# Performance work log

Hardware: AMD Instinct MI355X
Metric: run time of the kernel (lower is better)

The kernel has to match this reference:

```python
import jax, jax.numpy as jnp
import numpy as np

B, N, NE = 2, 10000, 320000
ND, ED = 128, 128
EPS = 1e-5


def _mlp(x, w1, b1, w2, b2, g, beta):
    # Linear -> SiLU -> Linear -> LayerNorm (MLP with n_hidden=1, layer_norm=True)
    h = jax.nn.silu(x @ w1 + b1)
    y = h @ w2 + b2
    mu = jnp.mean(y, axis=-1, keepdims=True)
    var = jnp.mean((y - mu) ** 2, axis=-1, keepdims=True)
    return (y - mu) * jax.lax.rsqrt(var + EPS) * g + beta


def setup_inputs() -> dict:
    key = jax.random.key(0)
    ks = jax.random.split(key, 16)
    V = jax.random.normal(ks[0], (B, N, ND), dtype=jnp.float32)
    E = jax.random.normal(ks[1], (B, NE, ED), dtype=jnp.float32)
    edges = jax.random.randint(ks[2], (B, NE, 2), 0, N, dtype=jnp.int32)
    inv = jax.random.bernoulli(ks[3], 0.01, (B, NE, 1))
    edges = jnp.where(inv, jnp.int32(-1), edges)

    def lin(k, fan_in, fan_out):
        kw, kb = jax.random.split(k)
        lim = 1.0 / np.sqrt(fan_in)
        w = jax.random.uniform(kw, (fan_in, fan_out), jnp.float32, -lim, lim)
        b = jax.random.uniform(kb, (fan_out,), jnp.float32, -lim, lim)
        return w, b

    fe_w1, fe_b1 = lin(ks[4], 2 * ND + ED, ND)   # f_edge: hidden=node_dim
    fe_w2, fe_b2 = lin(ks[5], ND, ED)
    fn_w1, fn_b1 = lin(ks[6], ND + ED, ND)       # f_node: hidden=node_dim
    fn_w2, fn_b2 = lin(ks[7], ND, ND)
    return {
        "V": V, "E": E, "edges": edges,
        "fe_w1": fe_w1, "fe_b1": fe_b1, "fe_w2": fe_w2, "fe_b2": fe_b2,
        "fe_g": jnp.ones((ED,), jnp.float32), "fe_beta": jnp.zeros((ED,), jnp.float32),
        "fn_w1": fn_w1, "fn_b1": fn_b1, "fn_w2": fn_w2, "fn_b2": fn_b2,
        "fn_g": jnp.ones((ND,), jnp.float32), "fn_beta": jnp.zeros((ND,), jnp.float32),
    }


def reference(V, E, edges, fe_w1, fe_b1, fe_w2, fe_b2, fe_g, fe_beta,
              fn_w1, fn_b1, fn_w2, fn_b2, fn_g, fn_beta):
    valid = jnp.all(edges >= 0, axis=-1)              # [B, NE]
    safe = jnp.clip(edges, 0, N - 1)                  # [B, NE, 2]
    bidx = jnp.arange(B)[:, None]
    S = V[bidx, safe[..., 0]]                         # [B, NE, ND] gather senders
    R = V[bidx, safe[..., 1]]                         # [B, NE, ND] gather receivers
    e_new = _mlp(jnp.concatenate([S, R, E], axis=-1), fe_w1, fe_b1, fe_w2, fe_b2, fe_g, fe_beta)
    e_new = e_new * valid[..., None]

    # scatter_mean over receiver index (invalid edges still counted, clamped to idx 0,
    # contributing zeros — matches torch scatter_mean with count.clamp(min=1))
    seg = (safe[..., 1] + bidx * N).reshape(-1)       # [B*NE]
    sums = jax.ops.segment_sum(e_new.reshape(-1, ED), seg, num_segments=B * N)
    cnt = jax.ops.segment_sum(jnp.ones((B * NE,), jnp.float32), seg, num_segments=B * N)
    agg = (sums / jnp.maximum(cnt, 1.0)[:, None]).reshape(B, N, ED)

    v_new = _mlp(jnp.concatenate([V, agg], axis=-1), fn_w1, fn_b1, fn_w2, fn_b2, fn_g, fn_beta)
    return V + v_new, E + e_new
```

## Files before the change

kernel.cpp:

```cpp
#include <hip/hip_runtime.h>

typedef float f32x4 __attribute__((ext_vector_type(4)));
typedef __bf16 bf16x8 __attribute__((ext_vector_type(8)));

constexpr int BATCH = 2;
constexpr int NNODE = 10000;
constexpr int NEDGE = 320000;
constexpr int D = 128;

constexpr size_t WS_SUMS = 0;
constexpr size_t WS_CNT  = 10240000;
constexpr size_t WS_W1E  = 10320000;
constexpr size_t WS_W2E  = 10418304;
constexpr size_t WS_W1N  = 10451072;
constexpr size_t WS_W2N  = 10516608;

__device__ __forceinline__ f32x4 mfma16(bf16x8 a, bf16x8 b, f32x4 c) {
    return __builtin_amdgcn_mfma_f32_16x16x32_bf16(a, b, c, 0, 0, 0);
}
__device__ __forceinline__ __bf16 tobf(float x) { return (__bf16)x; }
__device__ __forceinline__ bf16x8 cvt8(float4 a, float4 b) {
    bf16x8 r;
    r[0]=tobf(a.x); r[1]=tobf(a.y); r[2]=tobf(a.z); r[3]=tobf(a.w);
    r[4]=tobf(b.x); r[5]=tobf(b.y); r[6]=tobf(b.z); r[7]=tobf(b.w);
    return r;
}
__device__ __forceinline__ bf16x8 cvt8s(float4 a, float4 b, float s) {
    bf16x8 r;
    r[0]=tobf(a.x*s); r[1]=tobf(a.y*s); r[2]=tobf(a.z*s); r[3]=tobf(a.w*s);
    r[4]=tobf(b.x*s); r[5]=tobf(b.y*s); r[6]=tobf(b.z*s); r[7]=tobf(b.w*s);
    return r;
}
__device__ __forceinline__ float silu(float x) {
    float t = __builtin_amdgcn_exp2f(x * -1.44269504f);
    return x * __builtin_amdgcn_rcpf(1.0f + t);
}

__global__ void gnn_pack_kernel(const float* __restrict__ fe_w1, const float* __restrict__ fe_w2,
                                const float* __restrict__ fn_w1, const float* __restrict__ fn_w2,
                                ushort* __restrict__ w1e, ushort* __restrict__ w2e,
                                ushort* __restrict__ w1n, ushort* __restrict__ w2n) {
    int t = blockIdx.x * blockDim.x + threadIdx.x;
    const float* src; ushort* dst; int lt;
    if      (t <  6144) { src = fe_w1; dst = w1e; lt = t;         }
    else if (t <  8192) { src = fe_w2; dst = w2e; lt = t - 6144;  }
    else if (t < 12288) { src = fn_w1; dst = w1n; lt = t - 8192;  }
    else if (t < 14336) { src = fn_w2; dst = w2n; lt = t - 12288; }
    else return;
    int lane = lt & 63, ct = (lt >> 6) & 7, kb = lt >> 9;
    int n  = ct * 16 + (lane & 15);
    int k0 = kb * 32 + (lane >> 4) * 8;
    ushort tmp[8];
#pragma unroll
    for (int j = 0; j < 8; j++)
        tmp[j] = __builtin_bit_cast(ushort, tobf(src[(size_t)(k0 + j) * 128 + n]));
    uint4 pk;
    pk.x = tmp[0] | ((uint)tmp[1] << 16); pk.y = tmp[2] | ((uint)tmp[3] << 16);
    pk.z = tmp[4] | ((uint)tmp[5] << 16); pk.w = tmp[6] | ((uint)tmp[7] << 16);
    *(uint4*)(dst + (size_t)lt * 8) = pk;
}

__global__ void gnn_cnt_kernel(const int* __restrict__ edges, unsigned* __restrict__ cnt) {
    int t = blockIdx.x * blockDim.x + threadIdx.x;
    if (t >= BATCH * NEDGE) return;
    int er = edges[2 * t + 1];
    int b  = (t >= NEDGE) ? 1 : 0;
    int r  = min(max(er, 0), NNODE - 1);
    atomicAdd(&cnt[b * NNODE + r], 1u);
}

__launch_bounds__(512, 2)
__global__ void gnn_edge_kernel(const float* __restrict__ V, const float* __restrict__ E,
                                const int* __restrict__ edges,
                                const float* __restrict__ b1, const float* __restrict__ b2,
                                const float* __restrict__ g, const float* __restrict__ beta,
                                const ushort* __restrict__ w1p, const ushort* __restrict__ w2p,
                                float* __restrict__ sums, float* __restrict__ E_out) {
    __shared__ __align__(16) ushort lds[(98304 + 32768) / 2];
    const int tid = threadIdx.x;
    const int wave = tid >> 6, lane = tid & 63;
    const int quad = lane >> 4, c16 = lane & 15;

    {
        const uint4* s4 = (const uint4*)w1p;
        uint4* d4 = (uint4*)lds;
#pragma unroll
        for (int i = 0; i < 12; i++) d4[tid + i * 512] = s4[tid + i * 512];
    }
    __syncthreads();

    float b1v[8], b2v[8], gv[8], bev[8];
#pragma unroll
    for (int ct = 0; ct < 8; ct++) {
        int cg = ct * 16 + c16;
        b1v[ct] = b1[cg]; b2v[ct] = b2[cg]; gv[ct] = g[cg]; bev[ct] = beta[cg];
    }
    ushort* hslab = lds + 49152 + wave * 2048;

    for (int tile = blockIdx.x; tile < (BATCH * NEDGE) / 256; tile += gridDim.x) {
        const int row0 = tile * 256;
        const int bb = (row0 >= NEDGE) ? 1 : 0;
        const int wr0 = row0 + wave * 32;

        const float* pA[2][3];
#pragma unroll
        for (int rt = 0; rt < 2; rt++) {
            int ge = wr0 + rt * 16 + c16;
            int es = edges[2 * ge], er = edges[2 * ge + 1];
            int s = min(max(es, 0), NNODE - 1), r = min(max(er, 0), NNODE - 1);
            pA[rt][0] = V + ((size_t)bb * NNODE + s) * D;
            pA[rt][1] = V + ((size_t)bb * NNODE + r) * D;
            pA[rt][2] = E + (size_t)ge * D;
        }

        f32x4 acc1[2][8];
        const f32x4 fz = {0.f, 0.f, 0.f, 0.f};
#pragma unroll
        for (int rt = 0; rt < 2; rt++)
#pragma unroll
            for (int ct = 0; ct < 8; ct++) acc1[rt][ct] = fz;

#pragma unroll
        for (int kb = 0; kb < 12; kb++) {
            const int part = kb >> 2;
            const int kloc = (kb & 3) * 32 + quad * 8;
            bf16x8 a[2];
#pragma unroll
            for (int rt = 0; rt < 2; rt++) {
                const float* p = pA[rt][part] + kloc;
                float4 x0 = *(const float4*)p;
                float4 x1 = *(const float4*)(p + 4);
                a[rt] = cvt8(x0, x1);
            }
#pragma unroll
            for (int ct = 0; ct < 8; ct++) {
                bf16x8 bf = ((const bf16x8*)lds)[(kb * 8 + ct) * 64 + lane];
                acc1[0][ct] = mfma16(a[0], bf, acc1[0][ct]);
                acc1[1][ct] = mfma16(a[1], bf, acc1[1][ct]);
            }
        }

#pragma unroll
        for (int rt = 0; rt < 2; rt++) {
#pragma unroll
            for (int ct = 0; ct < 8; ct++)
#pragma unroll
                for (int i = 0; i < 4; i++) {
                    float x = acc1[rt][ct][i] + b1v[ct];
                    float h = silu(x);
                    int hrow = quad * 4 + i;
                    int boff = hrow * 256 + ((2 * (ct * 16 + c16)) ^ ((hrow & 7) << 4));
                    hslab[boff >> 1] = __builtin_bit_cast(ushort, tobf(h));
                }

            f32x4 acc2[8];
#pragma unroll
            for (int ct = 0; ct < 8; ct++) acc2[ct] = fz;

#pragma unroll
            for (int kb2 = 0; kb2 < 4; kb2++) {
                int boff = c16 * 256 + ((2 * (kb2 * 32 + quad * 8)) ^ ((c16 & 7) << 4));
                bf16x8 a2 = *(const bf16x8*)((const char*)hslab + boff);
#pragma unroll
                for (int ct = 0; ct < 8; ct++) {
                    bf16x8 bf = *(const bf16x8*)(w2p + ((size_t)((kb2 * 8 + ct) * 64 + lane)) * 8);
                    acc2[ct] = mfma16(a2, bf, acc2[ct]);
                }
            }

            float sm[4] = {0,0,0,0}, sq[4] = {0,0,0,0};
#pragma unroll
            for (int ct = 0; ct < 8; ct++)
#pragma unroll
                for (int i = 0; i < 4; i++) {
                    float y = acc2[ct][i] + b2v[ct];
                    acc2[ct][i] = y; sm[i] += y; sq[i] += y * y;
                }
#pragma unroll
            for (int m = 1; m < 16; m <<= 1)
#pragma unroll
                for (int i = 0; i < 4; i++) {
                    sm[i] += __shfl_xor(sm[i], m, 64);
                    sq[i] += __shfl_xor(sq[i], m, 64);
                }
            float mu[4], rstd[4];
#pragma unroll
            for (int i = 0; i < 4; i++) {
                mu[i] = sm[i] * (1.0f / 128.0f);
                float var = sq[i] * (1.0f / 128.0f) - mu[i] * mu[i];
                rstd[i] = __builtin_amdgcn_rsqf(var + 1e-5f);
            }

            size_t eb[4], sb[4]; bool val[4];
#pragma unroll
            for (int i = 0; i < 4; i++) {
                int geo = row0 + wave * 32 + rt * 16 + quad * 4 + i;
                int es = edges[2 * geo], er = edges[2 * geo + 1];
                val[i] = (es >= 0) && (er >= 0);
                int r = min(max(er, 0), NNODE - 1);
                eb[i] = (size_t)geo * D;
                sb[i] = ((size_t)bb * NNODE + r) * D;
            }
#pragma unroll
            for (int ct = 0; ct < 8; ct++) {
                int cg = ct * 16 + c16;
#pragma unroll
                for (int i = 0; i < 4; i++) {
                    float e = (acc2[ct][i] - mu[i]) * rstd[i] * gv[ct] + bev[ct];
                    e = val[i] ? e : 0.0f;
                    E_out[eb[i] + cg] = E[eb[i] + cg] + e;
                    if (val[i]) unsafeAtomicAdd(&sums[sb[i] + cg], e);
                }
            }
        }
    }
}

__launch_bounds__(512, 2)
__global__ void gnn_node_kernel(const float* __restrict__ V,
                                const float* __restrict__ sums, const unsigned* __restrict__ cnt,
                                const float* __restrict__ b1, const float* __restrict__ b2,
                                const float* __restrict__ g, const float* __restrict__ beta,
                                const ushort* __restrict__ w1p, const ushort* __restrict__ w2p,
                                float* __restrict__ V_out) {
    __shared__ __align__(16) ushort lds[(65536 + 32768) / 2];
    const int tid = threadIdx.x;
    const int wave = tid >> 6, lane = tid & 63;
    const int quad = lane >> 4, c16 = lane & 15;
    const int TOT = BATCH * NNODE;

    {
        const uint4* s4 = (const uint4*)w1p;
        uint4* d4 = (uint4*)lds;
#pragma unroll
        for (int i = 0; i < 8; i++) d4[tid + i * 512] = s4[tid + i * 512];
    }
    __syncthreads();

    float b1v[8], b2v[8], gv[8], bev[8];
#pragma unroll
    for (int ct = 0; ct < 8; ct++) {
        int cg = ct * 16 + c16;
        b1v[ct] = b1[cg]; b2v[ct] = b2[cg]; gv[ct] = g[cg]; bev[ct] = beta[cg];
    }
    ushort* hslab = lds + 32768 + wave * 2048;

    for (int tile = blockIdx.x; tile * 256 < TOT; tile += gridDim.x) {
        const int row0 = tile * 256;
        const int wr0 = row0 + wave * 32;

        const float* pV[2]; const float* pG[2]; float rinv[2];
#pragma unroll
        for (int rt = 0; rt < 2; rt++) {
            int grow = wr0 + rt * 16 + c16;
            int gc = min(grow, TOT - 1);
            pV[rt] = V    + (size_t)gc * D;
            pG[rt] = sums + (size_t)gc * D;
            rinv[rt] = __builtin_amdgcn_rcpf(fmaxf((float)cnt[gc], 1.0f));
        }

        f32x4 acc1[2][8];
        const f32x4 fz = {0.f, 0.f, 0.f, 0.f};
#pragma unroll
        for (int rt = 0; rt < 2; rt++)
#pragma unroll
            for (int ct = 0; ct < 8; ct++) acc1[rt][ct] = fz;

#pragma unroll
        for (int kb = 0; kb < 8; kb++) {
            const int part = kb >> 2;
            const int kloc = (kb & 3) * 32 + quad * 8;
            bf16x8 a[2];
#pragma unroll
            for (int rt = 0; rt < 2; rt++) {
                const float* p = (part == 0 ? pV[rt] : pG[rt]) + kloc;
                float4 x0 = *(const float4*)p;
                float4 x1 = *(const float4*)(p + 4);
                a[rt] = (part == 0) ? cvt8(x0, x1) : cvt8s(x0, x1, rinv[rt]);
            }
#pragma unroll
            for (int ct = 0; ct < 8; ct++) {
                bf16x8 bf = ((const bf16x8*)lds)[(kb * 8 + ct) * 64 + lane];
                acc1[0][ct] = mfma16(a[0], bf, acc1[0][ct]);
                acc1[1][ct] = mfma16(a[1], bf, acc1[1][ct]);
            }
        }

#pragma unroll
        for (int rt = 0; rt < 2; rt++) {
#pragma unroll
            for (int ct = 0; ct < 8; ct++)
#pragma unroll
                for (int i = 0; i < 4; i++) {
                    float x = acc1[rt][ct][i] + b1v[ct];
                    float h = silu(x);
                    int hrow = quad * 4 + i;
                    int boff = hrow * 256 + ((2 * (ct * 16 + c16)) ^ ((hrow & 7) << 4));
                    hslab[boff >> 1] = __builtin_bit_cast(ushort, tobf(h));
                }

            f32x4 acc2[8];
#pragma unroll
            for (int ct = 0; ct < 8; ct++) acc2[ct] = fz;
#pragma unroll
            for (int kb2 = 0; kb2 < 4; kb2++) {
                int boff = c16 * 256 + ((2 * (kb2 * 32 + quad * 8)) ^ ((c16 & 7) << 4));
                bf16x8 a2 = *(const bf16x8*)((const char*)hslab + boff);
#pragma unroll
                for (int ct = 0; ct < 8; ct++) {
                    bf16x8 bf = *(const bf16x8*)(w2p + ((size_t)((kb2 * 8 + ct) * 64 + lane)) * 8);
                    acc2[ct] = mfma16(a2, bf, acc2[ct]);
                }
            }

            float sm[4] = {0,0,0,0}, sq[4] = {0,0,0,0};
#pragma unroll
            for (int ct = 0; ct < 8; ct++)
#pragma unroll
                for (int i = 0; i < 4; i++) {
                    float y = acc2[ct][i] + b2v[ct];
                    acc2[ct][i] = y; sm[i] += y; sq[i] += y * y;
                }
#pragma unroll
            for (int m = 1; m < 16; m <<= 1)
#pragma unroll
                for (int i = 0; i < 4; i++) {
                    sm[i] += __shfl_xor(sm[i], m, 64);
                    sq[i] += __shfl_xor(sq[i], m, 64);
                }
            float mu[4], rstd[4];
#pragma unroll
            for (int i = 0; i < 4; i++) {
                mu[i] = sm[i] * (1.0f / 128.0f);
                float var = sq[i] * (1.0f / 128.0f) - mu[i] * mu[i];
                rstd[i] = __builtin_amdgcn_rsqf(var + 1e-5f);
            }
#pragma unroll
            for (int ct = 0; ct < 8; ct++) {
                int cg = ct * 16 + c16;
#pragma unroll
                for (int i = 0; i < 4; i++) {
                    int geo = row0 + wave * 32 + rt * 16 + quad * 4 + i;
                    if (geo < TOT) {
                        float vn = (acc2[ct][i] - mu[i]) * rstd[i] * gv[ct] + bev[ct];
                        V_out[(size_t)geo * D + cg] = V[(size_t)geo * D + cg] + vn;
                    }
                }
            }
        }
    }
}

extern "C" void kernel_launch(void* const* d_in, const int* in_sizes, int n_in,
                              void* d_out, int out_size, void* d_ws, size_t ws_size,
                              hipStream_t stream) {
    const float* V     = (const float*)d_in[0];
    const float* E     = (const float*)d_in[1];
    const int*   edges = (const int*)d_in[2];
    const float* fe_w1 = (const float*)d_in[3];
    const float* fe_b1 = (const float*)d_in[4];
    const float* fe_w2 = (const float*)d_in[5];
    const float* fe_b2 = (const float*)d_in[6];
    const float* fe_g  = (const float*)d_in[7];
    const float* fe_be = (const float*)d_in[8];
    const float* fn_w1 = (const float*)d_in[9];
    const float* fn_b1 = (const float*)d_in[10];
    const float* fn_w2 = (const float*)d_in[11];
    const float* fn_b2 = (const float*)d_in[12];
    const float* fn_g  = (const float*)d_in[13];
    const float* fn_be = (const float*)d_in[14];

    char* ws = (char*)d_ws;
    float*    sums = (float*)(ws + WS_SUMS);
    unsigned* cnt  = (unsigned*)(ws + WS_CNT);
    ushort*   w1e  = (ushort*)(ws + WS_W1E);
    ushort*   w2e  = (ushort*)(ws + WS_W2E);
    ushort*   w1n  = (ushort*)(ws + WS_W1N);
    ushort*   w2n  = (ushort*)(ws + WS_W2N);

    float* V_out = (float*)d_out;
    float* E_out = V_out + (size_t)BATCH * NNODE * D;

    hipMemsetAsync(d_ws, 0, WS_W1E, stream);
    gnn_pack_kernel<<<28, 512, 0, stream>>>(fe_w1, fe_w2, fn_w1, fn_w2, w1e, w2e, w1n, w2n);
    gnn_cnt_kernel<<<(BATCH * NEDGE) / 512, 512, 0, stream>>>(edges, cnt);
    gnn_edge_kernel<<<256, 512, 0, stream>>>(V, E, edges, fe_b1, fe_b2, fe_g, fe_be,
                                             w1e, w2e, sums, E_out);
    gnn_node_kernel<<<79, 512, 0, stream>>>(V, sums, cnt, fn_b1, fn_b2, fn_g, fn_be,
                                            w1n, w2n, V_out);
}
```

Before: 790.4 us.

## Replace float atomic scatter-mean with CSR edge lists and gather aggregation

The edge kernel no longer does per-element float atomicAdd into node sums. Instead, the edges are bucketed by receiver through a count pass, a single-block prefix scan and an atomic scatter into an edge list. The edge kernel stages masked e_new through LDS, writes E_out with coalesced float4 stores, and optionally stores a bf16 copy of e_new. A new per-node gather kernel sums each node's edges and divides by the count, and the edge kernel moves to 1024-thread blocks with 512-row tiles. The aim is to remove the heavy atomic contention and scattered writes, at the cost of extra passes and memory traffic, plus reduced precision because e_new is rounded to bf16 before it is added into E_out.

```diff
diff --git a/kernel.cpp b/kernel.cpp
--- a/kernel.cpp
+++ b/kernel.cpp
@@ -7,13 +7,20 @@
 constexpr int NNODE = 10000;
 constexpr int NEDGE = 320000;
 constexpr int D = 128;
-
-constexpr size_t WS_SUMS = 0;
-constexpr size_t WS_CNT  = 10240000;
-constexpr size_t WS_W1E  = 10320000;
-constexpr size_t WS_W2E  = 10418304;
-constexpr size_t WS_W1N  = 10451072;
-constexpr size_t WS_W2N  = 10516608;
+constexpr int TOTN = BATCH * NNODE;
+constexpr int TOTE = BATCH * NEDGE;
+
+constexpr size_t WS_CNT   = 0;
+constexpr size_t WS_OFF   = 80000;
+constexpr size_t WS_CUR   = 160000;
+constexpr size_t WS_ELIST = 240000;
+constexpr size_t WS_AGG   = 2800000;
+constexpr size_t WS_W1E   = 13040000;
+constexpr size_t WS_W2E   = 13138304;
+constexpr size_t WS_W1N   = 13171072;
+constexpr size_t WS_W2N   = 13236608;
+constexpr size_t WS_ENEW  = 13269376;
+constexpr size_t WS_NEED_ENEW = WS_ENEW + (size_t)TOTE * D * 2;
 
 __device__ __forceinline__ f32x4 mfma16(bf16x8 a, bf16x8 b, f32x4 c) {
     return __builtin_amdgcn_mfma_f32_16x16x32_bf16(a, b, c, 0, 0, 0);
@@ -23,12 +30,6 @@
     bf16x8 r;
     r[0]=tobf(a.x); r[1]=tobf(a.y); r[2]=tobf(a.z); r[3]=tobf(a.w);
     r[4]=tobf(b.x); r[5]=tobf(b.y); r[6]=tobf(b.z); r[7]=tobf(b.w);
-    return r;
-}
-__device__ __forceinline__ bf16x8 cvt8s(float4 a, float4 b, float s) {
-    bf16x8 r;
-    r[0]=tobf(a.x*s); r[1]=tobf(a.y*s); r[2]=tobf(a.z*s); r[3]=tobf(a.w*s);
-    r[4]=tobf(b.x*s); r[5]=tobf(b.y*s); r[6]=tobf(b.z*s); r[7]=tobf(b.w*s);
     return r;
 }
 __device__ __forceinline__ float silu(float x) {
@@ -62,21 +63,62 @@
 
 __global__ void gnn_cnt_kernel(const int* __restrict__ edges, unsigned* __restrict__ cnt) {
     int t = blockIdx.x * blockDim.x + threadIdx.x;
-    if (t >= BATCH * NEDGE) return;
+    if (t >= TOTE) return;
     int er = edges[2 * t + 1];
     int b  = (t >= NEDGE) ? 1 : 0;
     int r  = min(max(er, 0), NNODE - 1);
     atomicAdd(&cnt[b * NNODE + r], 1u);
 }
 
-__launch_bounds__(512, 2)
+__global__ void gnn_scan_kernel(const unsigned* __restrict__ cnt,
+                                unsigned* __restrict__ off, unsigned* __restrict__ cur) {
+    __shared__ unsigned s[1024];
+    const int t = threadIdx.x;
+    const int CH = 20;
+    unsigned loc[CH];
+    unsigned sum = 0;
+    int i0 = t * CH;
+#pragma unroll
+    for (int j = 0; j < CH; j++) {
+        int i = i0 + j;
+        unsigned v = (i < TOTN) ? cnt[i] : 0u;
+        loc[j] = sum; sum += v;
+    }
+    s[t] = sum;
+    __syncthreads();
+    for (int d = 1; d < 1024; d <<= 1) {
+        unsigned v = (t >= d) ? s[t - d] : 0u;
+        __syncthreads();
+        s[t] += v;
+        __syncthreads();
+    }
+    unsigned base = (t > 0) ? s[t - 1] : 0u;
+#pragma unroll
+    for (int j = 0; j < CH; j++) {
+        int i = i0 + j;
+        if (i < TOTN) { off[i] = base + loc[j]; cur[i] = base + loc[j]; }
+    }
+}
+
+__global__ void gnn_scatter_kernel(const int* __restrict__ edges,
+                                   unsigned* __restrict__ cur, unsigned* __restrict__ elist) {
+    int t = blockIdx.x * blockDim.x + threadIdx.x;
+    if (t >= TOTE) return;
+    int er = edges[2 * t + 1];
+    int b  = (t >= NEDGE) ? 1 : 0;
+    int r  = min(max(er, 0), NNODE - 1);
+    unsigned pos = atomicAdd(&cur[b * NNODE + r], 1u);
+    elist[pos] = (unsigned)t;
+}
+
+__launch_bounds__(1024, 4)
 __global__ void gnn_edge_kernel(const float* __restrict__ V, const float* __restrict__ E,
                                 const int* __restrict__ edges,
                                 const float* __restrict__ b1, const float* __restrict__ b2,
                                 const float* __restrict__ g, const float* __restrict__ beta,
                                 const ushort* __restrict__ w1p, const ushort* __restrict__ w2p,
-                                float* __restrict__ sums, float* __restrict__ E_out) {
-    __shared__ __align__(16) ushort lds[(98304 + 32768) / 2];
+                                float* __restrict__ E_out, ushort* __restrict__ enewp) {
+    __shared__ __align__(16) ushort lds[81920];
     const int tid = threadIdx.x;
     const int wave = tid >> 6, lane = tid & 63;
     const int quad = lane >> 4, c16 = lane & 15;
@@ -85,7 +127,7 @@
         const uint4* s4 = (const uint4*)w1p;
         uint4* d4 = (uint4*)lds;
 #pragma unroll
-        for (int i = 0; i < 12; i++) d4[tid + i * 512] = s4[tid + i * 512];
+        for (int i = 0; i < 6; i++) d4[tid + i * 1024] = s4[tid + i * 1024];
     }
     __syncthreads();
 
@@ -97,12 +139,12 @@
     }
     ushort* hslab = lds + 49152 + wave * 2048;
 
-    for (int tile = blockIdx.x; tile < (BATCH * NEDGE) / 256; tile += gridDim.x) {
-        const int row0 = tile * 256;
+    for (int tile = blockIdx.x; tile < TOTE / 512; tile += gridDim.x) {
+        const int row0 = tile * 512;
         const int bb = (row0 >= NEDGE) ? 1 : 0;
         const int wr0 = row0 + wave * 32;
 
-        const float* pA[2][3];
+        const float* pA[2][3]; uint mask16[2];
 #pragma unroll
         for (int rt = 0; rt < 2; rt++) {
             int ge = wr0 + rt * 16 + c16;
@@ -111,6 +153,7 @@
             pA[rt][0] = V + ((size_t)bb * NNODE + s) * D;
             pA[rt][1] = V + ((size_t)bb * NNODE + r) * D;
             pA[rt][2] = E + (size_t)ge * D;
+            mask16[rt] = (uint)(__ballot(es >= 0 && er >= 0) & 0xffffu);
         }
 
         f32x4 acc1[2][8];
@@ -149,7 +192,7 @@
                     float x = acc1[rt][ct][i] + b1v[ct];
                     float h = silu(x);
                     int hrow = quad * 4 + i;
-                    int boff = hrow * 256 + ((2 * (ct * 16 + c16)) ^ ((hrow & 7) << 4));
+                    int boff = hrow * 256 + ((2 * (ct * 16 + c16)) ^ (hrow << 4));
                     hslab[boff >> 1] = __builtin_bit_cast(ushort, tobf(h));
                 }
 
@@ -159,7 +202,7 @@
 
 #pragma unroll
             for (int kb2 = 0; kb2 < 4; kb2++) {
-                int boff = c16 * 256 + ((2 * (kb2 * 32 + quad * 8)) ^ ((c16 & 7) << 4));
+                int boff = c16 * 256 + ((kb2 * 64 + quad * 16) ^ (c16 << 4));
                 bf16x8 a2 = *(const bf16x8*)((const char*)hslab + boff);
 #pragma unroll
                 for (int ct = 0; ct < 8; ct++) {
@@ -191,43 +234,109 @@
                 rstd[i] = __builtin_amdgcn_rsqf(var + 1e-5f);
             }
 
-            size_t eb[4], sb[4]; bool val[4];
-#pragma unroll
-            for (int i = 0; i < 4; i++) {
-                int geo = row0 + wave * 32 + rt * 16 + quad * 4 + i;
-                int es = edges[2 * geo], er = edges[2 * geo + 1];
-                val[i] = (es >= 0) && (er >= 0);
-                int r = min(max(er, 0), NNODE - 1);
-                eb[i] = (size_t)geo * D;
-                sb[i] = ((size_t)bb * NNODE + r) * D;
-            }
-#pragma unroll
-            for (int ct = 0; ct < 8; ct++) {
-                int cg = ct * 16 + c16;
+#pragma unroll
+            for (int ct = 0; ct < 8; ct++)
 #pragma unroll
                 for (int i = 0; i < 4; i++) {
                     float e = (acc2[ct][i] - mu[i]) * rstd[i] * gv[ct] + bev[ct];
-                    e = val[i] ? e : 0.0f;
-                    E_out[eb[i] + cg] = E[eb[i] + cg] + e;
-                    if (val[i]) unsafeAtomicAdd(&sums[sb[i] + cg], e);
-                }
-            }
-        }
+                    int row = quad * 4 + i;
+                    e = ((mask16[rt] >> row) & 1u) ? e : 0.0f;
+                    int boff = row * 256 + ((2 * (ct * 16 + c16)) ^ (row << 4));
+                    hslab[boff >> 1] = __builtin_bit_cast(ushort, tobf(e));
+                }
+
+            const int r = lane >> 2, seg = lane & 3;
+            const int ge = wr0 + rt * 16 + r;
+#pragma unroll
+            for (int j = 0; j < 4; j++) {
+                int cb = (seg * 16 + j * 64) ^ (r << 4);
+                bf16x8 ev = *(const bf16x8*)((const char*)hslab + r * 256 + cb);
+                size_t gbase = (size_t)ge * D + seg * 8 + j * 32;
+                float4 e0 = *(const float4*)(E + gbase);
+                float4 e1 = *(const float4*)(E + gbase + 4);
+                float4 o0, o1;
+                o0.x = e0.x + (float)ev[0]; o0.y = e0.y + (float)ev[1];
+                o0.z = e0.z + (float)ev[2]; o0.w = e0.w + (float)ev[3];
+                o1.x = e1.x + (float)ev[4]; o1.y = e1.y + (float)ev[5];
+                o1.z = e1.z + (float)ev[6]; o1.w = e1.w + (float)ev[7];
+                *(float4*)(E_out + gbase) = o0;
+                *(float4*)(E_out + gbase + 4) = o1;
+                if (enewp) *(bf16x8*)(enewp + gbase) = ev;
+            }
+        }
+    }
+}
+
+__launch_bounds__(256)
+__global__ void gnn_agg_kernel(const float* __restrict__ E, const float* __restrict__ E_out,
+                               const ushort* __restrict__ enewp,
+                               const unsigned* __restrict__ off, const unsigned* __restrict__ cnt,
+                               const unsigned* __restrict__ elist, float* __restrict__ agg) {
+    const int lane = threadIdx.x & 63;
+    const int wid = (blockIdx.x * blockDim.x + threadIdx.x) >> 6;
+    const int nw = (gridDim.x * blockDim.x) >> 6;
+    const int col = lane << 1;
+    for (int n = wid; n < TOTN; n += nw) {
+        unsigned base = off[n], c = cnt[n];
+        float a0 = 0.f, a1 = 0.f;
+        unsigned e = 0;
+        if (enewp) {
+            while (e + 8 <= c) {
+                unsigned id[8]; uint v[8];
+#pragma unroll
+                for (int k = 0; k < 8; k++) id[k] = elist[base + e + k];
+#pragma unroll
+                for (int k = 0; k < 8; k++) v[k] = *(const uint*)(enewp + (size_t)id[k] * D + col);
+#pragma unroll
+                for (int k = 0; k < 8; k++) {
+                    a0 += __builtin_bit_cast(float, v[k] << 16);
+                    a1 += __builtin_bit_cast(float, v[k] & 0xffff0000u);
+                }
+                e += 8;
+            }
+            for (; e < c; e++) {
+                unsigned id = elist[base + e];
+                uint v = *(const uint*)(enewp + (size_t)id * D + col);
+                a0 += __builtin_bit_cast(float, v << 16);
+                a1 += __builtin_bit_cast(float, v & 0xffff0000u);
+            }
+        } else {
+            while (e + 8 <= c) {
+                unsigned id[8]; float2 eo[8], ee[8];
+#pragma unroll
+                for (int k = 0; k < 8; k++) id[k] = elist[base + e + k];
+#pragma unroll
+                for (int k = 0; k < 8; k++) {
+                    eo[k] = *(const float2*)(E_out + (size_t)id[k] * D + col);
+                    ee[k] = *(const float2*)(E + (size_t)id[k] * D + col);
+                }
+#pragma unroll
+                for (int k = 0; k < 8; k++) { a0 += eo[k].x - ee[k].x; a1 += eo[k].y - ee[k].y; }
+                e += 8;
+            }
+            for (; e < c; e++) {
+                unsigned id = elist[base + e];
+                float2 eo = *(const float2*)(E_out + (size_t)id * D + col);
+                float2 ee = *(const float2*)(E + (size_t)id * D + col);
+                a0 += eo.x - ee.x; a1 += eo.y - ee.y;
+            }
+        }
+        float rinv = 1.0f / (float)max(c, 1u);
+        float2 outv; outv.x = a0 * rinv; outv.y = a1 * rinv;
+        *(float2*)(agg + (size_t)n * D + col) = outv;
     }
 }
 
 __launch_bounds__(512, 2)
-__global__ void gnn_node_kernel(const float* __restrict__ V,
-                                const float* __restrict__ sums, const unsigned* __restrict__ cnt,
+__global__ void gnn_node_kernel(const float* __restrict__ V, const float* __restrict__ agg,
                                 const float* __restrict__ b1, const float* __restrict__ b2,
                                 const float* __restrict__ g, const float* __restrict__ beta,
                                 const ushort* __restrict__ w1p, const ushort* __restrict__ w2p,
                                 float* __restrict__ V_out) {
-    __shared__ __align__(16) ushort lds[(65536 + 32768) / 2];
+    __shared__ __align__(16) ushort lds[49152];
     const int tid = threadIdx.x;
     const int wave = tid >> 6, lane = tid & 63;
     const int quad = lane >> 4, c16 = lane & 15;
-    const int TOT = BATCH * NNODE;
 
     {
         const uint4* s4 = (const uint4*)w1p;
@@ -245,18 +354,17 @@
     }
     ushort* hslab = lds + 32768 + wave * 2048;
 
-    for (int tile = blockIdx.x; tile * 256 < TOT; tile += gridDim.x) {
+    for (int tile = blockIdx.x; tile * 256 < TOTN; tile += gridDim.x) {
         const int row0 = tile * 256;
         const int wr0 = row0 + wave * 32;
 
-        const float* pV[2]; const float* pG[2]; float rinv[2];
+        const float* pV[2]; const float* pG[2];
 #pragma unroll
         for (int rt = 0; rt < 2; rt++) {
             int grow = wr0 + rt * 16 + c16;
-            int gc = min(grow, TOT - 1);
-            pV[rt] = V    + (size_t)gc * D;
-            pG[rt] = sums + (size_t)gc * D;
-            rinv[rt] = __builtin_amdgcn_rcpf(fmaxf((float)cnt[gc], 1.0f));
+            int gc = min(grow, TOTN - 1);
+            pV[rt] = V   + (size_t)gc * D;
+            pG[rt] = agg + (size_t)gc * D;
         }
 
         f32x4 acc1[2][8];
@@ -276,7 +384,7 @@
                 const float* p = (part == 0 ? pV[rt] : pG[rt]) + kloc;
                 float4 x0 = *(const float4*)p;
                 float4 x1 = *(const float4*)(p + 4);
-                a[rt] = (part == 0) ? cvt8(x0, x1) : cvt8s(x0, x1, rinv[rt]);
+                a[rt] = cvt8(x0, x1);
             }
 #pragma unroll
             for (int ct = 0; ct < 8; ct++) {
@@ -295,7 +403,7 @@
                     float x = acc1[rt][ct][i] + b1v[ct];
                     float h = silu(x);
                     int hrow = quad * 4 + i;
-                    int boff = hrow * 256 + ((2 * (ct * 16 + c16)) ^ ((hrow & 7) << 4));
+                    int boff = hrow * 256 + ((2 * (ct * 16 + c16)) ^ (hrow << 4));
                     hslab[boff >> 1] = __builtin_bit_cast(ushort, tobf(h));
                 }
 
@@ -304,7 +412,7 @@
             for (int ct = 0; ct < 8; ct++) acc2[ct] = fz;
 #pragma unroll
             for (int kb2 = 0; kb2 < 4; kb2++) {
-                int boff = c16 * 256 + ((2 * (kb2 * 32 + quad * 8)) ^ ((c16 & 7) << 4));
+                int boff = c16 * 256 + ((kb2 * 64 + quad * 16) ^ (c16 << 4));
                 bf16x8 a2 = *(const bf16x8*)((const char*)hslab + boff);
 #pragma unroll
                 for (int ct = 0; ct < 8; ct++) {
@@ -341,7 +449,7 @@
 #pragma unroll
                 for (int i = 0; i < 4; i++) {
                     int geo = row0 + wave * 32 + rt * 16 + quad * 4 + i;
-                    if (geo < TOT) {
+                    if (geo < TOTN) {
                         float vn = (acc2[ct][i] - mu[i]) * rstd[i] * gv[ct] + bev[ct];
                         V_out[(size_t)geo * D + cg] = V[(size_t)geo * D + cg] + vn;
                     }
@@ -371,21 +479,28 @@
     const float* fn_be = (const float*)d_in[14];
 
     char* ws = (char*)d_ws;
-    float*    sums = (float*)(ws + WS_SUMS);
-    unsigned* cnt  = (unsigned*)(ws + WS_CNT);
-    ushort*   w1e  = (ushort*)(ws + WS_W1E);
-    ushort*   w2e  = (ushort*)(ws + WS_W2E);
-    ushort*   w1n  = (ushort*)(ws + WS_W1N);
-    ushort*   w2n  = (ushort*)(ws + WS_W2N);
+    unsigned* cnt   = (unsigned*)(ws + WS_CNT);
+    unsigned* off   = (unsigned*)(ws + WS_OFF);
+    unsigned* cur   = (unsigned*)(ws + WS_CUR);
+    unsigned* elist = (unsigned*)(ws + WS_ELIST);
+    float*    agg   = (float*)(ws + WS_AGG);
+    ushort*   w1e   = (ushort*)(ws + WS_W1E);
+    ushort*   w2e   = (ushort*)(ws + WS_W2E);
+    ushort*   w1n   = (ushort*)(ws + WS_W1N);
+    ushort*   w2n   = (ushort*)(ws + WS_W2N);
+    ushort*   enewp = (ws_size >= WS_NEED_ENEW) ? (ushort*)(ws + WS_ENEW) : (ushort*)nullptr;
 
     float* V_out = (float*)d_out;
-    float* E_out = V_out + (size_t)BATCH * NNODE * D;
-
-    hipMemsetAsync(d_ws, 0, WS_W1E, stream);
+    float* E_out = V_out + (size_t)TOTN * D;
+
+    hipMemsetAsync(cnt, 0, TOTN * sizeof(unsigned), stream);
     gnn_pack_kernel<<<28, 512, 0, stream>>>(fe_w1, fe_w2, fn_w1, fn_w2, w1e, w2e, w1n, w2n);
-    gnn_cnt_kernel<<<(BATCH * NEDGE) / 512, 512, 0, stream>>>(edges, cnt);
-    gnn_edge_kernel<<<256, 512, 0, stream>>>(V, E, edges, fe_b1, fe_b2, fe_g, fe_be,
-                                             w1e, w2e, sums, E_out);
-    gnn_node_kernel<<<79, 512, 0, stream>>>(V, sums, cnt, fn_b1, fn_b2, fn_g, fn_be,
+    gnn_cnt_kernel<<<TOTE / 512, 512, 0, stream>>>(edges, cnt);
+    gnn_scan_kernel<<<1, 1024, 0, stream>>>(cnt, off, cur);
+    gnn_scatter_kernel<<<TOTE / 512, 512, 0, stream>>>(edges, cur, elist);
+    gnn_edge_kernel<<<256, 1024, 0, stream>>>(V, E, edges, fe_b1, fe_b2, fe_g, fe_be,
+                                              w1e, w2e, E_out, enewp);
+    gnn_agg_kernel<<<512, 256, 0, stream>>>(E, E_out, enewp, off, cnt, elist, agg);
+    gnn_node_kernel<<<79, 512, 0, stream>>>(V, agg, fn_b1, fn_b2, fn_g, fn_be,
                                             w1n, w2n, V_out);
 }
```

Result: slower. 1.311 ms (+65.9%).
